# Kernel tuning notes

Hardware: AMD Instinct MI355X
Metric: run time of the kernel (lower is better)

Reference implementation:

```python
import jax, jax.numpy as jnp
import numpy as np

N_NODES = 100000
N_EDGES = 1600000
IN_CH, HID_CH, OUT_CH = 128, 128, 64


def setup_inputs() -> dict:
    key = jax.random.key(0)
    ks = jax.random.split(key, 9)
    x = jax.random.normal(ks[0], (N_NODES, IN_CH), dtype=jnp.float32)
    edge_index = jax.random.randint(ks[1], (2, N_EDGES), 0, N_NODES, dtype=jnp.int64)
    def glorot(k, shape):
        fan_in = shape[1]
        return jax.random.normal(k, shape, dtype=jnp.float32) / jnp.sqrt(jnp.float32(fan_in))
    return {
        "x": x,
        "edge_index": edge_index,
        "W1_l": glorot(ks[2], (HID_CH, IN_CH)),
        "W1_r": glorot(ks[3], (HID_CH, IN_CH)),
        "b1": jnp.zeros((HID_CH,), jnp.float32),
        "W2_l": glorot(ks[4], (HID_CH, HID_CH)),
        "W2_r": glorot(ks[5], (HID_CH, HID_CH)),
        "b2": jnp.zeros((HID_CH,), jnp.float32),
        "W3_l": glorot(ks[6], (OUT_CH, HID_CH)),
        "W3_r": glorot(ks[7], (OUT_CH, HID_CH)),
        "b3": jnp.zeros((OUT_CH,), jnp.float32),
    }


def _sage_conv(x, src, dst, W_l, W_r, b):
    # PyG SAGEConv (aggr='mean', root_weight=True): out = lin_l(mean_j x_j) + lin_r(x_i)
    n = x.shape[0]
    msg = x[src]                                            # [E, C] gather at source
    agg = jax.ops.segment_sum(msg, dst, num_segments=n)     # [N, C] scatter-sum at dest
    cnt = jax.ops.segment_sum(jnp.ones((src.shape[0],), x.dtype), dst, num_segments=n)
    mean = agg / jnp.maximum(cnt, 1.0)[:, None]             # zero-in-degree nodes -> 0
    return mean @ W_l.T + x @ W_r.T + b


def reference(x, edge_index, W1_l, W1_r, b1, W2_l, W2_r, b2, W3_l, W3_r, b3):
    src, dst = edge_index[0], edge_index[1]
    h = jax.nn.relu(_sage_conv(x, src, dst, W1_l, W1_r, b1))
    # F.dropout with training=False is identity (eval mode)
    h = jax.nn.relu(_sage_conv(h, src, dst, W2_l, W2_r, b2))
    return _sage_conv(h, src, dst, W3_l, W3_r, b3)
```

## Files before the change

kernel.cpp:

```cpp
#include <hip/hip_runtime.h>
#include <hip/hip_bf16.h>
#include <cstddef>
#include <cstdint>

#define NBLK(n, b) (((n) + (b) - 1) / (b))

typedef __attribute__((ext_vector_type(8))) short short8;
typedef __attribute__((ext_vector_type(4))) float f32x4;
typedef __attribute__((ext_vector_type(2))) float f32x2;

__device__ inline unsigned short f2bf(float f) {
  union { float f; unsigned u; } v; v.f = f;
  unsigned u = v.u;
  u += 0x7FFFu + ((u >> 16) & 1u);
  return (unsigned short)(u >> 16);
}
__device__ inline float bflo(unsigned u) { union { unsigned u; float f; } v; v.u = u << 16; return v.f; }
__device__ inline float bfhi(unsigned u) { union { unsigned u; float f; } v; v.u = u & 0xFFFF0000u; return v.f; }

#define BSHIFT 9
#define BSIZE 512
#define CAPSHIFT 14
#define CAP 16384
#define ECHUNK 2048


__global__ __launch_bounds__(256) void k_cast(
    const float* __restrict__ x, unsigned* __restrict__ xT, int N,
    const float* __restrict__ W1l, const float* __restrict__ W1r, unsigned short* __restrict__ Wb1,
    const float* __restrict__ W2l, const float* __restrict__ W2r, unsigned short* __restrict__ Wb2,
    const float* __restrict__ W3l, const float* __restrict__ W3r, unsigned short* __restrict__ Wb3) {
  int t = threadIdx.x;
  int b = blockIdx.x;
  int gCast = (N * 64 + 255) >> 8;
  if (b < gCast) {
    int i = b * 256 + t;
    if (i < N * 64) {
      float2 v = *(const float2*)(x + (size_t)i * 2);
      int node = i >> 6, j = i & 63;
      xT[((size_t)(j >> 3) * N + node) * 8 + (j & 7)] =
          (unsigned)f2bf(v.x) | ((unsigned)f2bf(v.y) << 16);
    }
    return;
  }
  b -= gCast;
  int ii = b * 256 + t;
  const float *Wl, *Wr; unsigned short* Wb;
  if (ii < 128 * 256) { Wl = W1l; Wr = W1r; Wb = Wb1; }
  else if (ii < 256 * 256) { Wl = W2l; Wr = W2r; Wb = Wb2; ii -= 128 * 256; }
  else { Wl = W3l; Wr = W3r; Wb = Wb3; ii -= 256 * 256; }
  int nrow = ii >> 8, k = ii & 255;
  float v = (k < 128) ? Wr[nrow * 128 + k] : Wl[nrow * 128 + (k - 128)];
  Wb[ii] = f2bf(v);
}

__global__ __launch_bounds__(256) void k_scatter(
    const void* __restrict__ edges, int* __restrict__ bucketCursor,
    unsigned* __restrict__ bucketed, int E, int NB) {
  __shared__ int h[1024];
  __shared__ int base2[1024];
  int t = threadIdx.x;
  int b = blockIdx.x;

  const unsigned* e32 = (const unsigned*)edges;
  int is64 = 1;
#pragma unroll
  for (int i = 0; i < 16; ++i)
    if (e32[2 * i + 1] != 0u) is64 = 0;

  for (int i = t; i < NB; i += 256) h[i] = 0;
  __syncthreads();
  int base_e = b * ECHUNK;
  unsigned key[8];
  int bkt[8];
#pragma unroll
  for (int k = 0; k < 8; ++k) {
    int e = base_e + k * 256 + t;
    bkt[k] = -1;
    if (e < E) {
      int s, d;
      if (is64) {
        s = (int)((const long long*)edges)[e];
        d = (int)((const long long*)edges)[(size_t)E + e];
      } else {
        s = ((const int*)edges)[e];
        d = ((const int*)edges)[(size_t)E + e];
      }
      bkt[k] = d >> BSHIFT;
      key[k] = (unsigned)s | ((unsigned)(d & (BSIZE - 1)) << 17);
      atomicAdd(&h[bkt[k]], 1);
    }
  }
  __syncthreads();
  for (int i = t; i < NB; i += 256) {
    int c = h[i];
    base2[i] = c ? atomicAdd(&bucketCursor[i], c) : 0;
    h[i] = 0;
  }
  __syncthreads();
#pragma unroll
  for (int k = 0; k < 8; ++k) {
    if (bkt[k] >= 0) {
      int r = atomicAdd(&h[bkt[k]], 1);
      int pos = base2[bkt[k]] + r;
      if (pos < CAP)
        bucketed[((size_t)bkt[k] << CAPSHIFT) + pos] = key[k];
    }
  }
}

__global__ __launch_bounds__(256) void k_csr(const unsigned* __restrict__ bucketed,
                                             const int* __restrict__ bucketCursor,
                                             int* __restrict__ rowStart, int* __restrict__ deg,
                                             int* __restrict__ srcSorted, int N, int NB) {
  __shared__ int h[512];
  __shared__ int excl[512];
  __shared__ int sd[256];
  int b = blockIdx.x;
  int t = threadIdx.x;
  int nodeBase = b << BSHIFT;
  int nNode = min(BSIZE, N - nodeBase);
  int cnt = min(bucketCursor[b], CAP);
  size_t s0 = (size_t)b << CAPSHIFT;
  h[t * 2] = 0; h[t * 2 + 1] = 0;
  __syncthreads();
  for (int i = t; i < cnt; i += 256) {
    int ld = bucketed[s0 + i] >> 17;
    atomicAdd(&h[ld], 1);
  }
  __syncthreads();
  int a0 = h[t * 2], a1 = h[t * 2 + 1];
  int s = a0 + a1;
  sd[t] = s;
  __syncthreads();
  for (int off = 1; off < 256; off <<= 1) {
    int xv = (t >= off) ? sd[t - off] : 0;
    __syncthreads();
    sd[t] += xv;
    __syncthreads();
  }
  int run = sd[t] - s;
  excl[t * 2] = run;
  excl[t * 2 + 1] = run + a0;
  if (t * 2 < nNode) {
    rowStart[nodeBase + t * 2] = (int)s0 + run;
    deg[nodeBase + t * 2] = a0;
  }
  if (t * 2 + 1 < nNode) {
    rowStart[nodeBase + t * 2 + 1] = (int)s0 + run + a0;
    deg[nodeBase + t * 2 + 1] = a1;
  }
  h[t * 2] = 0; h[t * 2 + 1] = 0;
  __syncthreads();
  for (int i = t; i < cnt; i += 256) {
    unsigned u = bucketed[s0 + i];
    int ld = u >> 17;
    int r = atomicAdd(&h[ld], 1);
    srcSorted[s0 + excl[ld] + r] = (int)(u & 0x1FFFFu);
  }
}

__global__ __launch_bounds__(256) void k_agg_slice(
    const uint4* __restrict__ inT, const int* __restrict__ rowStart,
    const int* __restrict__ deg, const int* __restrict__ srcs,
    uint4* __restrict__ outT, int n) {
  int g = blockIdx.x & 7;
  int node = ((blockIdx.x >> 3) << 7) + (threadIdx.x >> 1);
  int h = threadIdx.x & 1;
  if (node >= n) return;
  int dg = deg[node];
  f32x2 acc0 = {0.f, 0.f}, acc1 = {0.f, 0.f}, acc2 = {0.f, 0.f}, acc3 = {0.f, 0.f};
  const uint4* base = inT + (size_t)g * n * 2 + h;
  if (dg > 0) {
    int r0 = rowStart[node];
    int r1 = r0 + dg;
    for (int b = r0; b < r1; b += 8) {
      int s[8];
      uint4 v[8];
#pragma unroll
      for (int i = 0; i < 8; ++i) s[i] = srcs[min(b + i, r1 - 1)] & 0x1FFFF;
#pragma unroll
      for (int i = 0; i < 8; ++i) v[i] = base[(size_t)s[i] * 2];
#pragma unroll
      for (int i = 0; i < 8; ++i) {
        if (b + i < r1) {
          f32x2 t0 = {bflo(v[i].x), bfhi(v[i].x)};
          f32x2 t1 = {bflo(v[i].y), bfhi(v[i].y)};
          f32x2 t2 = {bflo(v[i].z), bfhi(v[i].z)};
          f32x2 t3 = {bflo(v[i].w), bfhi(v[i].w)};
          acc0 += t0; acc1 += t1; acc2 += t2; acc3 += t3;
        }
      }
    }
  }
  float sc = 1.0f / (float)max(dg, 1);
  uint4 o;
  o.x = (unsigned)f2bf(acc0.x * sc) | ((unsigned)f2bf(acc0.y * sc) << 16);
  o.y = (unsigned)f2bf(acc1.x * sc) | ((unsigned)f2bf(acc1.y * sc) << 16);
  o.z = (unsigned)f2bf(acc2.x * sc) | ((unsigned)f2bf(acc2.y * sc) << 16);
  o.w = (unsigned)f2bf(acc3.x * sc) | ((unsigned)f2bf(acc3.y * sc) << 16);
  outT[((size_t)g * n + node) * 2 + h] = o;
}

template <int H, bool RELU>
__global__ __launch_bounds__(256) void k_gemm(
    const unsigned short* __restrict__ selfT, const unsigned short* __restrict__ meanT,
    const unsigned short* __restrict__ Wb, const float* __restrict__ bias,
    unsigned short* __restrict__ outT, int n) {
  constexpr int TN = H / 32;
  int lane = threadIdx.x & 63;
  int w = threadIdx.x >> 6;
  int wr = w & 1, wc = w >> 1;
  int nodeBase = blockIdx.x * 128 + wr * 64;
  int colBase = wc * (H / 2);
  int l15 = lane & 15, quad = lane >> 4;

  f32x4 acc[4][TN];
#pragma unroll
  for (int t = 0; t < 4; ++t)
#pragma unroll
    for (int j = 0; j < TN; ++j) acc[t][j] = (f32x4){0.f, 0.f, 0.f, 0.f};

#pragma unroll
  for (int c = 0; c < 8; ++c) {
    const unsigned short* A = (c < 4) ? selfT : meanT;
    int ko = (c & 3) * 32 + quad * 8;
    int gk = ko >> 4;
    int wo = ko & 15;
    short8 af[4], bfr[TN];
#pragma unroll
    for (int t = 0; t < 4; ++t) {
      int row = min(nodeBase + t * 16 + l15, n - 1);
      af[t] = *(const short8*)(A + ((size_t)gk * n + row) * 16 + wo);
    }
#pragma unroll
    for (int j = 0; j < TN; ++j) {
      int cn = colBase + j * 16 + l15;
      bfr[j] = *(const short8*)(Wb + (size_t)cn * 256 + c * 32 + quad * 8);
    }
#pragma unroll
    for (int t = 0; t < 4; ++t)
#pragma unroll
      for (int j = 0; j < TN; ++j)
        acc[t][j] = __builtin_amdgcn_mfma_f32_16x16x32_bf16(af[t], bfr[j], acc[t][j], 0, 0, 0);
  }

#pragma unroll
  for (int j = 0; j < TN; ++j) {
    int col = colBase + j * 16 + l15;
    int gc = col >> 4;
    float bv = bias[col];
#pragma unroll
    for (int t = 0; t < 4; ++t) {
#pragma unroll
      for (int r = 0; r < 4; ++r) {
        int row = nodeBase + t * 16 + quad * 4 + r;
        if (row < n) {
          float v = acc[t][j][r] + bv;
          if (RELU) v = fmaxf(v, 0.f);
          outT[((size_t)gc * n + row) * 16 + l15] = f2bf(v);
        }
      }
    }
  }
}

__global__ __launch_bounds__(256) void k_gemm3_both(
    const unsigned short* __restrict__ A,
    const unsigned short* __restrict__ Wb3,
    const float* __restrict__ bias,
    float* __restrict__ outp, unsigned short* __restrict__ y3T, int n) {
  int lane = threadIdx.x & 63;
  int w = threadIdx.x >> 6;
  int wr = w & 1, wc = w >> 1;
  int nodeBase = blockIdx.x * 128 + wr * 64;
  int l15 = lane & 15, quad = lane >> 4;
  int woff = wc ? 128 : 0;
  f32x4 acc[4][4];
#pragma unroll
  for (int t = 0; t < 4; ++t)
#pragma unroll
    for (int j = 0; j < 4; ++j) acc[t][j] = (f32x4){0.f, 0.f, 0.f, 0.f};
#pragma unroll
  for (int c = 0; c < 4; ++c) {
    int ko = c * 32 + quad * 8;
    int gk = ko >> 4;
    int wo = ko & 15;
    short8 af[4], bfr[4];
#pragma unroll
    for (int t = 0; t < 4; ++t) {
      int row = min(nodeBase + t * 16 + l15, n - 1);
      af[t] = *(const short8*)(A + ((size_t)gk * n + row) * 16 + wo);
    }
#pragma unroll
    for (int j = 0; j < 4; ++j) {
      int cn = j * 16 + l15;
      bfr[j] = *(const short8*)(Wb3 + (size_t)cn * 256 + woff + c * 32 + quad * 8);
    }
#pragma unroll
    for (int t = 0; t < 4; ++t)
#pragma unroll
      for (int j = 0; j < 4; ++j)
        acc[t][j] = __builtin_amdgcn_mfma_f32_16x16x32_bf16(af[t], bfr[j], acc[t][j], 0, 0, 0);
  }
#pragma unroll
  for (int j = 0; j < 4; ++j) {
    int col = j * 16 + l15;
    float bv = wc ? 0.f : bias[col];
#pragma unroll
    for (int t = 0; t < 4; ++t) {
#pragma unroll
      for (int r = 0; r < 4; ++r) {
        int row = nodeBase + t * 16 + quad * 4 + r;
        if (row < n) {
          float v = acc[t][j][r] + bv;
          if (wc) y3T[((size_t)j * n + row) * 16 + l15] = f2bf(v);
          else outp[(size_t)row * 64 + col] = v;
        }
      }
    }
  }
}

__global__ __launch_bounds__(256) void k_agg64_slice(
    const uint4* __restrict__ y3T, const int* __restrict__ rowStart,
    const int* __restrict__ deg, const int* __restrict__ srcs,
    float* __restrict__ outp, int n) {
  int g = blockIdx.x & 3;
  int node = ((blockIdx.x >> 2) << 7) + (threadIdx.x >> 1);
  int h = threadIdx.x & 1;
  if (node >= n) return;
  int dg = deg[node];
  if (dg == 0) return;
  int r0 = rowStart[node];
  int r1 = r0 + dg;
  f32x2 acc0 = {0.f, 0.f}, acc1 = {0.f, 0.f}, acc2 = {0.f, 0.f}, acc3 = {0.f, 0.f};
  const uint4* base = y3T + (size_t)g * n * 2 + h;
  for (int b = r0; b < r1; b += 8) {
    int s[8];
    uint4 v[8];
#pragma unroll
    for (int i = 0; i < 8; ++i) s[i] = srcs[min(b + i, r1 - 1)] & 0x1FFFF;
#pragma unroll
    for (int i = 0; i < 8; ++i) v[i] = base[(size_t)s[i] * 2];
#pragma unroll
    for (int i = 0; i < 8; ++i) {
      if (b + i < r1) {
        f32x2 t0 = {bflo(v[i].x), bfhi(v[i].x)};
        f32x2 t1 = {bflo(v[i].y), bfhi(v[i].y)};
        f32x2 t2 = {bflo(v[i].z), bfhi(v[i].z)};
        f32x2 t3 = {bflo(v[i].w), bfhi(v[i].w)};
        acc0 += t0; acc1 += t1; acc2 += t2; acc3 += t3;
      }
    }
  }
  float sc = 1.0f / (float)dg;
  float* op = outp + (size_t)node * 64 + g * 16 + h * 8;
  float4 a = *(float4*)op;
  float4 c = *(float4*)(op + 4);
  a.x += acc0.x * sc; a.y += acc0.y * sc; a.z += acc1.x * sc; a.w += acc1.y * sc;
  c.x += acc2.x * sc; c.y += acc2.y * sc; c.z += acc3.x * sc; c.w += acc3.y * sc;
  *(float4*)op = a;
  *(float4*)(op + 4) = c;
}


extern "C" void kernel_launch(void* const* d_in, const int* in_sizes, int n_in,
                              void* d_out, int out_size, void* d_ws, size_t ws_size,
                              hipStream_t stream) {
  (void)n_in; (void)out_size; (void)ws_size;
  const float* x = (const float*)d_in[0];
  const void* edges = d_in[1];
  const float* W1l = (const float*)d_in[2];
  const float* W1r = (const float*)d_in[3];
  const float* b1 = (const float*)d_in[4];
  const float* W2l = (const float*)d_in[5];
  const float* W2r = (const float*)d_in[6];
  const float* b2 = (const float*)d_in[7];
  const float* W3l = (const float*)d_in[8];
  const float* W3r = (const float*)d_in[9];
  const float* b3 = (const float*)d_in[10];
  float* out = (float*)d_out;

  const int N = in_sizes[0] / 128;
  const int E = in_sizes[1] / 2;
  const int NB = (N + BSIZE - 1) >> BSHIFT;

  char* ws = (char*)d_ws;
  size_t off = 0;
  auto alloc = [&](size_t bytes) -> char* {
    char* p = ws + off;
    off = (off + bytes + 255) & ~(size_t)255;
    return p;
  };
  int* bucketCursor = (int*)alloc((size_t)NB * 4);
  unsigned* bucketed = (unsigned*)alloc((size_t)NB * CAP * 4);
  int* rowStart = (int*)alloc((size_t)N * 4);
  int* deg = (int*)alloc((size_t)N * 4);
  int* srcSorted = (int*)alloc((size_t)NB * CAP * 4);
  unsigned short* xT = (unsigned short*)alloc((size_t)N * 128 * 2);
  unsigned short* meanT = (unsigned short*)alloc((size_t)N * 128 * 2);
  unsigned short* h1T = (unsigned short*)alloc((size_t)N * 128 * 2);
  unsigned short* h2T = (unsigned short*)alloc((size_t)N * 128 * 2);
  unsigned short* y3T = (unsigned short*)alloc((size_t)N * 64 * 2);
  unsigned short* Wb1 = (unsigned short*)alloc(128 * 256 * 2);
  unsigned short* Wb2 = (unsigned short*)alloc(128 * 256 * 2);
  unsigned short* Wb3 = (unsigned short*)alloc(64 * 256 * 2);

  int gCast = NBLK(N * 64, 256) + 320;
  int gE = NBLK(E, ECHUNK);
  int gRange = NBLK(N, 128);
  int gGemm = NBLK(N, 128);

  hipMemsetAsync(bucketCursor, 0, (size_t)NB * 4, stream);
  k_cast<<<gCast, 256, 0, stream>>>(x, (unsigned*)xT, N,
                                    W1l, W1r, Wb1, W2l, W2r, Wb2, W3l, W3r, Wb3);
  k_scatter<<<gE, 256, 0, stream>>>(edges, bucketCursor, bucketed, E, NB);
  k_csr<<<NB, 256, 0, stream>>>(bucketed, bucketCursor, rowStart, deg, srcSorted, N, NB);

  k_agg_slice<<<gRange * 8, 256, 0, stream>>>((const uint4*)xT, rowStart, deg, srcSorted,
                                              (uint4*)meanT, N);
  k_gemm<128, true><<<gGemm, 256, 0, stream>>>(xT, meanT, Wb1, b1, h1T, N);
  k_agg_slice<<<gRange * 8, 256, 0, stream>>>((const uint4*)h1T, rowStart, deg, srcSorted,
                                              (uint4*)meanT, N);
  k_gemm<128, true><<<gGemm, 256, 0, stream>>>(h1T, meanT, Wb2, b2, h2T, N);
  k_gemm3_both<<<gGemm, 256, 0, stream>>>(h2T, Wb3, b3, out, y3T, N);
  k_agg64_slice<<<gRange * 4, 256, 0, stream>>>((const uint4*)y3T, rowStart, deg, srcSorted,
                                                out, N);
}
```

Before: 525.0 us.

## Parallelize neighbor aggregation across edges with 16 lanes per node

The aggregation kernels now assign 16 lanes per node instead of 2. Lanes split the node's edges into 8 edge groups and the 2 halves of the 16-byte feature slice. Source indices are loaded cooperatively and distributed with shuffles, then partial sums are reduced with xor-shuffles before one lane group writes the result. This aims to expose more memory-level parallelism and shorten the serial per-node loop, since in-degree averages about 16. In exchange it launches 8x more blocks, wastes lanes on low-degree nodes, and adds shuffle reduction overhead.

```diff
diff --git a/kernel.cpp b/kernel.cpp
--- a/kernel.cpp
+++ b/kernel.cpp
@@ -7,7 +7,6 @@
 
 typedef __attribute__((ext_vector_type(8))) short short8;
 typedef __attribute__((ext_vector_type(4))) float f32x4;
-typedef __attribute__((ext_vector_type(2))) float f32x2;
 
 __device__ inline unsigned short f2bf(float f) {
   union { float f; unsigned u; } v; v.f = f;
@@ -165,41 +164,60 @@
     const int* __restrict__ deg, const int* __restrict__ srcs,
     uint4* __restrict__ outT, int n) {
   int g = blockIdx.x & 7;
-  int node = ((blockIdx.x >> 3) << 7) + (threadIdx.x >> 1);
-  int h = threadIdx.x & 1;
-  if (node >= n) return;
-  int dg = deg[node];
-  f32x2 acc0 = {0.f, 0.f}, acc1 = {0.f, 0.f}, acc2 = {0.f, 0.f}, acc3 = {0.f, 0.f};
-  const uint4* base = inT + (size_t)g * n * 2 + h;
-  if (dg > 0) {
-    int r0 = rowStart[node];
-    int r1 = r0 + dg;
-    for (int b = r0; b < r1; b += 8) {
-      int s[8];
-      uint4 v[8];
-#pragma unroll
-      for (int i = 0; i < 8; ++i) s[i] = srcs[min(b + i, r1 - 1)] & 0x1FFFF;
-#pragma unroll
-      for (int i = 0; i < 8; ++i) v[i] = base[(size_t)s[i] * 2];
-#pragma unroll
-      for (int i = 0; i < 8; ++i) {
-        if (b + i < r1) {
-          f32x2 t0 = {bflo(v[i].x), bfhi(v[i].x)};
-          f32x2 t1 = {bflo(v[i].y), bfhi(v[i].y)};
-          f32x2 t2 = {bflo(v[i].z), bfhi(v[i].z)};
-          f32x2 t3 = {bflo(v[i].w), bfhi(v[i].w)};
-          acc0 += t0; acc1 += t1; acc2 += t2; acc3 += t3;
-        }
+  int lane = threadIdx.x & 63;
+  int w = threadIdx.x >> 6;
+  int q = lane >> 4;
+  int l15 = lane & 15;
+  int eg = (lane >> 1) & 7;
+  int sub = lane & 1;
+  int node = (blockIdx.x >> 3) * 16 + w * 4 + q;
+  bool valid = node < n;
+  int nc = valid ? node : n - 1;
+  int r0 = rowStart[nc];
+  int dg = valid ? deg[nc] : 0;
+  int r1 = r0 + dg;
+  const uint4* bp = inT + (size_t)g * n * 2 + sub;
+  float acc[8];
+#pragma unroll
+  for (int k = 0; k < 8; ++k) acc[k] = 0.f;
+
+  for (int base = r0; base < r1; base += 32) {
+    int sv0 = srcs[min(base + l15, r1 - 1)];
+    int sv1 = srcs[min(base + 16 + l15, r1 - 1)];
+    uint4 v[4];
+    int e[4];
+#pragma unroll
+    for (int k = 0; k < 4; ++k) {
+      int s = __shfl((k < 2) ? sv0 : sv1, q * 16 + (k & 1) * 8 + eg);
+      v[k] = bp[(size_t)s * 2];
+      e[k] = base + k * 8 + eg;
+    }
+#pragma unroll
+    for (int k = 0; k < 4; ++k) {
+      if (e[k] < r1) {
+        acc[0] += bflo(v[k].x); acc[1] += bfhi(v[k].x);
+        acc[2] += bflo(v[k].y); acc[3] += bfhi(v[k].y);
+        acc[4] += bflo(v[k].z); acc[5] += bfhi(v[k].z);
+        acc[6] += bflo(v[k].w); acc[7] += bfhi(v[k].w);
       }
     }
   }
-  float sc = 1.0f / (float)max(dg, 1);
-  uint4 o;
-  o.x = (unsigned)f2bf(acc0.x * sc) | ((unsigned)f2bf(acc0.y * sc) << 16);
-  o.y = (unsigned)f2bf(acc1.x * sc) | ((unsigned)f2bf(acc1.y * sc) << 16);
-  o.z = (unsigned)f2bf(acc2.x * sc) | ((unsigned)f2bf(acc2.y * sc) << 16);
-  o.w = (unsigned)f2bf(acc3.x * sc) | ((unsigned)f2bf(acc3.y * sc) << 16);
-  outT[((size_t)g * n + node) * 2 + h] = o;
+
+#pragma unroll
+  for (int k = 0; k < 8; ++k) {
+    acc[k] += __shfl_xor(acc[k], 2);
+    acc[k] += __shfl_xor(acc[k], 4);
+    acc[k] += __shfl_xor(acc[k], 8);
+  }
+  if (eg == 0 && valid) {
+    float sc = 1.0f / (float)max(dg, 1);
+    uint4 o;
+    o.x = (unsigned)f2bf(acc[0] * sc) | ((unsigned)f2bf(acc[1] * sc) << 16);
+    o.y = (unsigned)f2bf(acc[2] * sc) | ((unsigned)f2bf(acc[3] * sc) << 16);
+    o.z = (unsigned)f2bf(acc[4] * sc) | ((unsigned)f2bf(acc[5] * sc) << 16);
+    o.w = (unsigned)f2bf(acc[6] * sc) | ((unsigned)f2bf(acc[7] * sc) << 16);
+    outT[((size_t)g * n + node) * 2 + sub] = o;
+  }
 }
 
 template <int H, bool RELU>
@@ -327,41 +345,61 @@
     const int* __restrict__ deg, const int* __restrict__ srcs,
     float* __restrict__ outp, int n) {
   int g = blockIdx.x & 3;
-  int node = ((blockIdx.x >> 2) << 7) + (threadIdx.x >> 1);
-  int h = threadIdx.x & 1;
-  if (node >= n) return;
-  int dg = deg[node];
-  if (dg == 0) return;
-  int r0 = rowStart[node];
+  int lane = threadIdx.x & 63;
+  int w = threadIdx.x >> 6;
+  int q = lane >> 4;
+  int l15 = lane & 15;
+  int eg = (lane >> 1) & 7;
+  int sub = lane & 1;
+  int node = (blockIdx.x >> 2) * 16 + w * 4 + q;
+  bool valid = node < n;
+  int nc = valid ? node : n - 1;
+  int r0 = rowStart[nc];
+  int dg = valid ? deg[nc] : 0;
   int r1 = r0 + dg;
-  f32x2 acc0 = {0.f, 0.f}, acc1 = {0.f, 0.f}, acc2 = {0.f, 0.f}, acc3 = {0.f, 0.f};
-  const uint4* base = y3T + (size_t)g * n * 2 + h;
-  for (int b = r0; b < r1; b += 8) {
-    int s[8];
-    uint4 v[8];
-#pragma unroll
-    for (int i = 0; i < 8; ++i) s[i] = srcs[min(b + i, r1 - 1)] & 0x1FFFF;
-#pragma unroll
-    for (int i = 0; i < 8; ++i) v[i] = base[(size_t)s[i] * 2];
-#pragma unroll
-    for (int i = 0; i < 8; ++i) {
-      if (b + i < r1) {
-        f32x2 t0 = {bflo(v[i].x), bfhi(v[i].x)};
-        f32x2 t1 = {bflo(v[i].y), bfhi(v[i].y)};
-        f32x2 t2 = {bflo(v[i].z), bfhi(v[i].z)};
-        f32x2 t3 = {bflo(v[i].w), bfhi(v[i].w)};
-        acc0 += t0; acc1 += t1; acc2 += t2; acc3 += t3;
+  const uint4* bp = y3T + (size_t)g * n * 2 + sub;
+  float acc[8];
+#pragma unroll
+  for (int k = 0; k < 8; ++k) acc[k] = 0.f;
+
+  for (int base = r0; base < r1; base += 32) {
+    int sv0 = srcs[min(base + l15, r1 - 1)];
+    int sv1 = srcs[min(base + 16 + l15, r1 - 1)];
+    uint4 v[4];
+    int e[4];
+#pragma unroll
+    for (int k = 0; k < 4; ++k) {
+      int s = __shfl((k < 2) ? sv0 : sv1, q * 16 + (k & 1) * 8 + eg);
+      v[k] = bp[(size_t)s * 2];
+      e[k] = base + k * 8 + eg;
+    }
+#pragma unroll
+    for (int k = 0; k < 4; ++k) {
+      if (e[k] < r1) {
+        acc[0] += bflo(v[k].x); acc[1] += bfhi(v[k].x);
+        acc[2] += bflo(v[k].y); acc[3] += bfhi(v[k].y);
+        acc[4] += bflo(v[k].z); acc[5] += bfhi(v[k].z);
+        acc[6] += bflo(v[k].w); acc[7] += bfhi(v[k].w);
       }
     }
   }
-  float sc = 1.0f / (float)dg;
-  float* op = outp + (size_t)node * 64 + g * 16 + h * 8;
-  float4 a = *(float4*)op;
-  float4 c = *(float4*)(op + 4);
-  a.x += acc0.x * sc; a.y += acc0.y * sc; a.z += acc1.x * sc; a.w += acc1.y * sc;
-  c.x += acc2.x * sc; c.y += acc2.y * sc; c.z += acc3.x * sc; c.w += acc3.y * sc;
-  *(float4*)op = a;
-  *(float4*)(op + 4) = c;
+
+#pragma unroll
+  for (int k = 0; k < 8; ++k) {
+    acc[k] += __shfl_xor(acc[k], 2);
+    acc[k] += __shfl_xor(acc[k], 4);
+    acc[k] += __shfl_xor(acc[k], 8);
+  }
+  if (eg == 0 && valid && dg > 0) {
+    float sc = 1.0f / (float)dg;
+    float* op = outp + (size_t)node * 64 + g * 16 + sub * 8;
+    float4 a = *(float4*)op;
+    float4 c = *(float4*)(op + 4);
+    a.x += acc[0] * sc; a.y += acc[1] * sc; a.z += acc[2] * sc; a.w += acc[3] * sc;
+    c.x += acc[4] * sc; c.y += acc[5] * sc; c.z += acc[6] * sc; c.w += acc[7] * sc;
+    *(float4*)op = a;
+    *(float4*)(op + 4) = c;
+  }
 }
 
 
@@ -409,7 +447,8 @@
 
   int gCast = NBLK(N * 64, 256) + 320;
   int gE = NBLK(E, ECHUNK);
-  int gRange = NBLK(N, 128);
+  int gAgg = NBLK(N, 16) * 8;
+  int gAgg64 = NBLK(N, 16) * 4;
   int gGemm = NBLK(N, 128);
 
   hipMemsetAsync(bucketCursor, 0, (size_t)NB * 4, stream);
@@ -418,13 +457,13 @@
   k_scatter<<<gE, 256, 0, stream>>>(edges, bucketCursor, bucketed, E, NB);
   k_csr<<<NB, 256, 0, stream>>>(bucketed, bucketCursor, rowStart, deg, srcSorted, N, NB);
 
-  k_agg_slice<<<gRange * 8, 256, 0, stream>>>((const uint4*)xT, rowStart, deg, srcSorted,
-                                              (uint4*)meanT, N);
+  k_agg_slice<<<gAgg, 256, 0, stream>>>((const uint4*)xT, rowStart, deg, srcSorted,
+                                        (uint4*)meanT, N);
   k_gemm<128, true><<<gGemm, 256, 0, stream>>>(xT, meanT, Wb1, b1, h1T, N);
-  k_agg_slice<<<gRange * 8, 256, 0, stream>>>((const uint4*)h1T, rowStart, deg, srcSorted,
-                                              (uint4*)meanT, N);
+  k_agg_slice<<<gAgg, 256, 0, stream>>>((const uint4*)h1T, rowStart, deg, srcSorted,
+                                        (uint4*)meanT, N);
   k_gemm<128, true><<<gGemm, 256, 0, stream>>>(h1T, meanT, Wb2, b2, h2T, N);
   k_gemm3_both<<<gGemm, 256, 0, stream>>>(h2T, Wb3, b3, out, y3T, N);
-  k_agg64_slice<<<gRange * 4, 256, 0, stream>>>((const uint4*)y3T, rowStart, deg, srcSorted,
-                                                out, N);
-}
+  k_agg64_slice<<<gAgg64, 256, 0, stream>>>((const uint4*)y3T, rowStart, deg, srcSorted,
+                                            out, N);
+}
```

New measurement: 475.5 us. -9.4%, faster.

## Sort nodes by degree within buckets and use one thread per node for aggregation

Applied to the files above, without the earlier changes.

The CSR build now also produces a per-bucket permutation of nodes ordered by in-degree, computed with a shared-memory counting sort. The aggregation kernels map one thread to one node, taking nodes in permuted order so that threads in a wavefront have similar degrees and diverge less. Each thread now gathers a 32-byte slice per edge with two 16-byte loads, processing two edges per iteration instead of batching eight. In exchange, fewer loads are in flight per thread, adjacent lanes no longer coalesce into contiguous 32-byte segments, and output writes are scattered through the permutation.

```diff
diff --git a/kernel.cpp b/kernel.cpp
--- a/kernel.cpp
+++ b/kernel.cpp
@@ -7,7 +7,6 @@
 
 typedef __attribute__((ext_vector_type(8))) short short8;
 typedef __attribute__((ext_vector_type(4))) float f32x4;
-typedef __attribute__((ext_vector_type(2))) float f32x2;
 
 __device__ inline unsigned short f2bf(float f) {
   union { float f; unsigned u; } v; v.f = f;
@@ -17,6 +16,14 @@
 }
 __device__ inline float bflo(unsigned u) { union { unsigned u; float f; } v; v.u = u << 16; return v.f; }
 __device__ inline float bfhi(unsigned u) { union { unsigned u; float f; } v; v.u = u & 0xFFFF0000u; return v.f; }
+
+__device__ inline void add8(float* a, uint4 v) {
+  a[0] += bflo(v.x); a[1] += bfhi(v.x);
+  a[2] += bflo(v.y); a[3] += bfhi(v.y);
+  a[4] += bflo(v.z); a[5] += bfhi(v.z);
+  a[6] += bflo(v.w); a[7] += bfhi(v.w);
+}
+
 
 #define BSHIFT 9
 #define BSIZE 512
@@ -112,7 +119,8 @@
 __global__ __launch_bounds__(256) void k_csr(const unsigned* __restrict__ bucketed,
                                              const int* __restrict__ bucketCursor,
                                              int* __restrict__ rowStart, int* __restrict__ deg,
-                                             int* __restrict__ srcSorted, int N, int NB) {
+                                             int* __restrict__ srcSorted, int* __restrict__ perm,
+                                             int N, int NB) {
   __shared__ int h[512];
   __shared__ int excl[512];
   __shared__ int sd[256];
@@ -158,48 +166,122 @@
     int r = atomicAdd(&h[ld], 1);
     srcSorted[s0 + excl[ld] + r] = (int)(u & 0x1FFFFu);
   }
+  __syncthreads();
+  if (t < 64) sd[t] = 0;
+  __syncthreads();
+  if (t * 2 < nNode) atomicAdd(&sd[min(a0, 63)], 1);
+  if (t * 2 + 1 < nNode) atomicAdd(&sd[min(a1, 63)], 1);
+  __syncthreads();
+  if (t == 0) {
+    int r2 = 0;
+    for (int i = 0; i < 64; ++i) { int c = sd[i]; excl[i] = r2; r2 += c; }
+  }
+  __syncthreads();
+  if (t * 2 < nNode) {
+    int p = atomicAdd(&excl[min(a0, 63)], 1);
+    perm[nodeBase + p] = nodeBase + t * 2;
+  }
+  if (t * 2 + 1 < nNode) {
+    int p = atomicAdd(&excl[min(a1, 63)], 1);
+    perm[nodeBase + p] = nodeBase + t * 2 + 1;
+  }
 }
 
 __global__ __launch_bounds__(256) void k_agg_slice(
     const uint4* __restrict__ inT, const int* __restrict__ rowStart,
     const int* __restrict__ deg, const int* __restrict__ srcs,
-    uint4* __restrict__ outT, int n) {
+    const int* __restrict__ perm, uint4* __restrict__ outT, int n) {
   int g = blockIdx.x & 7;
-  int node = ((blockIdx.x >> 3) << 7) + (threadIdx.x >> 1);
-  int h = threadIdx.x & 1;
-  if (node >= n) return;
+  int idx = (blockIdx.x >> 3) * 256 + threadIdx.x;
+  if (idx >= n) return;
+  int node = perm[idx];
+  int r0 = rowStart[node];
   int dg = deg[node];
-  f32x2 acc0 = {0.f, 0.f}, acc1 = {0.f, 0.f}, acc2 = {0.f, 0.f}, acc3 = {0.f, 0.f};
-  const uint4* base = inT + (size_t)g * n * 2 + h;
-  if (dg > 0) {
-    int r0 = rowStart[node];
-    int r1 = r0 + dg;
-    for (int b = r0; b < r1; b += 8) {
-      int s[8];
-      uint4 v[8];
-#pragma unroll
-      for (int i = 0; i < 8; ++i) s[i] = srcs[min(b + i, r1 - 1)] & 0x1FFFF;
-#pragma unroll
-      for (int i = 0; i < 8; ++i) v[i] = base[(size_t)s[i] * 2];
-#pragma unroll
-      for (int i = 0; i < 8; ++i) {
-        if (b + i < r1) {
-          f32x2 t0 = {bflo(v[i].x), bfhi(v[i].x)};
-          f32x2 t1 = {bflo(v[i].y), bfhi(v[i].y)};
-          f32x2 t2 = {bflo(v[i].z), bfhi(v[i].z)};
-          f32x2 t3 = {bflo(v[i].w), bfhi(v[i].w)};
-          acc0 += t0; acc1 += t1; acc2 += t2; acc3 += t3;
-        }
-      }
-    }
-  }
+  const uint4* bp = inT + (size_t)g * n * 2;
+  float acc[16];
+#pragma unroll
+  for (int k = 0; k < 16; ++k) acc[k] = 0.f;
+
+  int e = 0;
+  for (; e + 2 <= dg; e += 2) {
+    int s0 = srcs[r0 + e];
+    int s1 = srcs[r0 + e + 1];
+    uint4 a0 = bp[(size_t)s0 * 2];
+    uint4 a1 = bp[(size_t)s0 * 2 + 1];
+    uint4 b0 = bp[(size_t)s1 * 2];
+    uint4 b1 = bp[(size_t)s1 * 2 + 1];
+    add8(acc, a0); add8(acc + 8, a1);
+    add8(acc, b0); add8(acc + 8, b1);
+  }
+  if (e < dg) {
+    int s0 = srcs[r0 + e];
+    uint4 a0 = bp[(size_t)s0 * 2];
+    uint4 a1 = bp[(size_t)s0 * 2 + 1];
+    add8(acc, a0); add8(acc + 8, a1);
+  }
+
   float sc = 1.0f / (float)max(dg, 1);
-  uint4 o;
-  o.x = (unsigned)f2bf(acc0.x * sc) | ((unsigned)f2bf(acc0.y * sc) << 16);
-  o.y = (unsigned)f2bf(acc1.x * sc) | ((unsigned)f2bf(acc1.y * sc) << 16);
-  o.z = (unsigned)f2bf(acc2.x * sc) | ((unsigned)f2bf(acc2.y * sc) << 16);
-  o.w = (unsigned)f2bf(acc3.x * sc) | ((unsigned)f2bf(acc3.y * sc) << 16);
-  outT[((size_t)g * n + node) * 2 + h] = o;
+  uint4 o0, o1;
+  o0.x = (unsigned)f2bf(acc[0] * sc) | ((unsigned)f2bf(acc[1] * sc) << 16);
+  o0.y = (unsigned)f2bf(acc[2] * sc) | ((unsigned)f2bf(acc[3] * sc) << 16);
+  o0.z = (unsigned)f2bf(acc[4] * sc) | ((unsigned)f2bf(acc[5] * sc) << 16);
+  o0.w = (unsigned)f2bf(acc[6] * sc) | ((unsigned)f2bf(acc[7] * sc) << 16);
+  o1.x = (unsigned)f2bf(acc[8] * sc) | ((unsigned)f2bf(acc[9] * sc) << 16);
+  o1.y = (unsigned)f2bf(acc[10] * sc) | ((unsigned)f2bf(acc[11] * sc) << 16);
+  o1.z = (unsigned)f2bf(acc[12] * sc) | ((unsigned)f2bf(acc[13] * sc) << 16);
+  o1.w = (unsigned)f2bf(acc[14] * sc) | ((unsigned)f2bf(acc[15] * sc) << 16);
+  outT[((size_t)g * n + node) * 2] = o0;
+  outT[((size_t)g * n + node) * 2 + 1] = o1;
+}
+
+__global__ __launch_bounds__(256) void k_agg64_slice(
+    const uint4* __restrict__ y3T, const int* __restrict__ rowStart,
+    const int* __restrict__ deg, const int* __restrict__ srcs,
+    const int* __restrict__ perm, float* __restrict__ outp, int n) {
+  int g = blockIdx.x & 3;
+  int idx = (blockIdx.x >> 2) * 256 + threadIdx.x;
+  if (idx >= n) return;
+  int node = perm[idx];
+  int dg = deg[node];
+  if (dg == 0) return;
+  int r0 = rowStart[node];
+  const uint4* bp = y3T + (size_t)g * n * 2;
+  float acc[16];
+#pragma unroll
+  for (int k = 0; k < 16; ++k) acc[k] = 0.f;
+
+  int e = 0;
+  for (; e + 2 <= dg; e += 2) {
+    int s0 = srcs[r0 + e];
+    int s1 = srcs[r0 + e + 1];
+    uint4 a0 = bp[(size_t)s0 * 2];
+    uint4 a1 = bp[(size_t)s0 * 2 + 1];
+    uint4 b0 = bp[(size_t)s1 * 2];
+    uint4 b1 = bp[(size_t)s1 * 2 + 1];
+    add8(acc, a0); add8(acc + 8, a1);
+    add8(acc, b0); add8(acc + 8, b1);
+  }
+  if (e < dg) {
+    int s0 = srcs[r0 + e];
+    uint4 a0 = bp[(size_t)s0 * 2];
+    uint4 a1 = bp[(size_t)s0 * 2 + 1];
+    add8(acc, a0); add8(acc + 8, a1);
+  }
+
+  float sc = 1.0f / (float)dg;
+  float* op = outp + (size_t)node * 64 + g * 16;
+  float4 v0 = *(float4*)op;
+  float4 v1 = *(float4*)(op + 4);
+  float4 v2 = *(float4*)(op + 8);
+  float4 v3 = *(float4*)(op + 12);
+  v0.x += acc[0] * sc; v0.y += acc[1] * sc; v0.z += acc[2] * sc; v0.w += acc[3] * sc;
+  v1.x += acc[4] * sc; v1.y += acc[5] * sc; v1.z += acc[6] * sc; v1.w += acc[7] * sc;
+  v2.x += acc[8] * sc; v2.y += acc[9] * sc; v2.z += acc[10] * sc; v2.w += acc[11] * sc;
+  v3.x += acc[12] * sc; v3.y += acc[13] * sc; v3.z += acc[14] * sc; v3.w += acc[15] * sc;
+  *(float4*)op = v0;
+  *(float4*)(op + 4) = v1;
+  *(float4*)(op + 8) = v2;
+  *(float4*)(op + 12) = v3;
 }
 
 template <int H, bool RELU>
@@ -320,48 +402,6 @@
       }
     }
   }
-}
-
-__global__ __launch_bounds__(256) void k_agg64_slice(
-    const uint4* __restrict__ y3T, const int* __restrict__ rowStart,
-    const int* __restrict__ deg, const int* __restrict__ srcs,
-    float* __restrict__ outp, int n) {
-  int g = blockIdx.x & 3;
-  int node = ((blockIdx.x >> 2) << 7) + (threadIdx.x >> 1);
-  int h = threadIdx.x & 1;
-  if (node >= n) return;
-  int dg = deg[node];
-  if (dg == 0) return;
-  int r0 = rowStart[node];
-  int r1 = r0 + dg;
-  f32x2 acc0 = {0.f, 0.f}, acc1 = {0.f, 0.f}, acc2 = {0.f, 0.f}, acc3 = {0.f, 0.f};
-  const uint4* base = y3T + (size_t)g * n * 2 + h;
-  for (int b = r0; b < r1; b += 8) {
-    int s[8];
-    uint4 v[8];
-#pragma unroll
-    for (int i = 0; i < 8; ++i) s[i] = srcs[min(b + i, r1 - 1)] & 0x1FFFF;
-#pragma unroll
-    for (int i = 0; i < 8; ++i) v[i] = base[(size_t)s[i] * 2];
-#pragma unroll
-    for (int i = 0; i < 8; ++i) {
-      if (b + i < r1) {
-        f32x2 t0 = {bflo(v[i].x), bfhi(v[i].x)};
-        f32x2 t1 = {bflo(v[i].y), bfhi(v[i].y)};
-        f32x2 t2 = {bflo(v[i].z), bfhi(v[i].z)};
-        f32x2 t3 = {bflo(v[i].w), bfhi(v[i].w)};
-        acc0 += t0; acc1 += t1; acc2 += t2; acc3 += t3;
-      }
-    }
-  }
-  float sc = 1.0f / (float)dg;
-  float* op = outp + (size_t)node * 64 + g * 16 + h * 8;
-  float4 a = *(float4*)op;
-  float4 c = *(float4*)(op + 4);
-  a.x += acc0.x * sc; a.y += acc0.y * sc; a.z += acc1.x * sc; a.w += acc1.y * sc;
-  c.x += acc2.x * sc; c.y += acc2.y * sc; c.z += acc3.x * sc; c.w += acc3.y * sc;
-  *(float4*)op = a;
-  *(float4*)(op + 4) = c;
 }
 
 
@@ -397,6 +437,7 @@
   unsigned* bucketed = (unsigned*)alloc((size_t)NB * CAP * 4);
   int* rowStart = (int*)alloc((size_t)N * 4);
   int* deg = (int*)alloc((size_t)N * 4);
+  int* perm = (int*)alloc((size_t)N * 4);
   int* srcSorted = (int*)alloc((size_t)NB * CAP * 4);
   unsigned short* xT = (unsigned short*)alloc((size_t)N * 128 * 2);
   unsigned short* meanT = (unsigned short*)alloc((size_t)N * 128 * 2);
@@ -409,22 +450,23 @@
 
   int gCast = NBLK(N * 64, 256) + 320;
   int gE = NBLK(E, ECHUNK);
-  int gRange = NBLK(N, 128);
+  int gAgg = NBLK(N, 256) * 8;
+  int gAgg64 = NBLK(N, 256) * 4;
   int gGemm = NBLK(N, 128);
 
   hipMemsetAsync(bucketCursor, 0, (size_t)NB * 4, stream);
   k_cast<<<gCast, 256, 0, stream>>>(x, (unsigned*)xT, N,
                                     W1l, W1r, Wb1, W2l, W2r, Wb2, W3l, W3r, Wb3);
   k_scatter<<<gE, 256, 0, stream>>>(edges, bucketCursor, bucketed, E, NB);
-  k_csr<<<NB, 256, 0, stream>>>(bucketed, bucketCursor, rowStart, deg, srcSorted, N, NB);
-
-  k_agg_slice<<<gRange * 8, 256, 0, stream>>>((const uint4*)xT, rowStart, deg, srcSorted,
-                                              (uint4*)meanT, N);
+  k_csr<<<NB, 256, 0, stream>>>(bucketed, bucketCursor, rowStart, deg, srcSorted, perm, N, NB);
+
+  k_agg_slice<<<gAgg, 256, 0, stream>>>((const uint4*)xT, rowStart, deg, srcSorted, perm,
+                                        (uint4*)meanT, N);
   k_gemm<128, true><<<gGemm, 256, 0, stream>>>(xT, meanT, Wb1, b1, h1T, N);
-  k_agg_slice<<<gRange * 8, 256, 0, stream>>>((const uint4*)h1T, rowStart, deg, srcSorted,
-                                              (uint4*)meanT, N);
+  k_agg_slice<<<gAgg, 256, 0, stream>>>((const uint4*)h1T, rowStart, deg, srcSorted, perm,
+                                        (uint4*)meanT, N);
   k_gemm<128, true><<<gGemm, 256, 0, stream>>>(h1T, meanT, Wb2, b2, h2T, N);
   k_gemm3_both<<<gGemm, 256, 0, stream>>>(h2T, Wb3, b3, out, y3T, N);
-  k_agg64_slice<<<gRange * 4, 256, 0, stream>>>((const uint4*)y3T, rowStart, deg, srcSorted,
-                                                out, N);
-}
+  k_agg64_slice<<<gAgg64, 256, 0, stream>>>((const uint4*)y3T, rowStart, deg, srcSorted, perm,
+                                            out, N);
+}
```

Result: slower. 731.7 us (+39.4%).
